# Kernel optimization log

Measured on AMD Instinct MI355X. Metric: run time of the kernel, lower is better.

## Reference

```python
import jax, jax.numpy as jnp
import numpy as np

EPS = 1e-5
PATCH_HW = 4096   # 64*64
STEP = 2048


def _conv(x, w, b=None, stride=(1, 1), pad=((0, 0), (0, 0))):
    y = jax.lax.conv_general_dilated(x, w, stride, pad,
                                     dimension_numbers=('NCHW', 'OIHW', 'NCHW'))
    return y if b is None else y + b[None, :, None, None]


def _bn(x, s, b, m, v):
    # inference-mode BatchNorm2d
    inv = s * jax.lax.rsqrt(v + EPS)
    return (x - m[None, :, None, None]) * inv[None, :, None, None] + b[None, :, None, None]


def _forward(x, w1, b1, w2, b2, w3, b3,
             c5a_w, bn5a_s, bn5a_b, bn5a_m, bn5a_v,
             c5c_w, bn5c_s, bn5c_b, bn5c_m, bn5c_v,
             c51_w, bn51_s, bn51_b, bn51_m, bn51_v,
             c52_w, bn52_s, bn52_b, bn52_m, bn52_v,
             pam_q_w, pam_q_b, pam_k_w, pam_k_b, pam_v_w, pam_v_b,
             pam_gamma, cam_gamma, c8_w, c8_b):
    B, L = x.shape
    need = PATCH_HW - (L % PATCH_HW)          # torch pads even when L%hw==0; L chosen non-multiple
    xp = jnp.pad(x, ((0, 0), (0, need)))
    nw = (xp.shape[1] - PATCH_HW) // STEP + 1  # sliding windows (unfold)
    idx = jnp.arange(nw)[:, None] * STEP + jnp.arange(PATCH_HW)[None, :]
    # [nw,1,64,64].reshape(1,1,hw,nw) in torch is a pure row-major reshape
    c_in = xp[:, idx].reshape(B, 1, PATCH_HW, nw)   # [B,1,4096,61]
    # FCN backbone
    h = jax.nn.relu(_conv(c_in, w1, b1, (4, 4), ((4, 4), (4, 4))))   # [B,128,1025,16]
    h = jax.nn.relu(_conv(h, w2, b2, (2, 2), ((2, 2), (2, 2))))      # [B,256,513,8]
    h = jax.nn.relu(_conv(h, w3, b3, (1, 1), ((1, 1), (1, 1))))      # [B,128,513,8]
    p1 = ((1, 1), (1, 1))
    # PAM branch
    feat1 = jax.nn.relu(_bn(_conv(h, c5a_w, None, (1, 1), p1), bn5a_s, bn5a_b, bn5a_m, bn5a_v))
    _, C, Hh, Ww = feat1.shape
    N = Hh * Ww                                    # 4104
    q = _conv(feat1, pam_q_w, pam_q_b).reshape(B, -1, N)   # [B,4,N]
    k = _conv(feat1, pam_k_w, pam_k_b).reshape(B, -1, N)
    attn = jax.nn.softmax(jnp.einsum('bdn,bdm->bnm', q, k), axis=-1)   # [B,N,N], no scaling (as in source)
    v = _conv(feat1, pam_v_w, pam_v_b).reshape(B, C, N)
    sa = pam_gamma * jnp.einsum('bcj,bij->bci', v, attn).reshape(feat1.shape) + feat1
    sa_conv = jax.nn.relu(_bn(_conv(sa, c51_w, None, (1, 1), p1), bn51_s, bn51_b, bn51_m, bn51_v))
    # CAM branch
    feat2 = jax.nn.relu(_bn(_conv(h, c5c_w, None, (1, 1), p1), bn5c_s, bn5c_b, bn5c_m, bn5c_v))
    Xf = feat2.reshape(B, C, N)
    energy = jnp.einsum('bcn,bdn->bcd', Xf, Xf)                 # [B,C,C]
    cattn = jax.nn.softmax(jnp.max(energy, -1, keepdims=True) - energy, axis=-1)  # max-subtract inversion
    sc = cam_gamma * jnp.einsum('bcd,bdn->bcn', cattn, Xf).reshape(feat2.shape) + feat2
    sc_conv = jax.nn.relu(_bn(_conv(sc, c52_w, None, (1, 1), p1), bn52_s, bn52_b, bn52_m, bn52_v))
    # fused head output (conv8; dropout is identity in eval)
    out = _conv(sa_conv + sc_conv, c8_w, c8_b)                  # [B,nclass,513,8]
    return out[:, None]                                          # torch.stack adds a dim -> [B,1,nclass,513,8]


def setup_inputs() -> dict:
    key = jax.random.key(0)
    it = iter(jax.random.split(key, 40))
    def rn(shape, s=0.05):
        return jax.random.normal(next(it), shape, jnp.float32) * s
    d = {}
    d['x'] = jax.random.normal(next(it), (4, 126975), jnp.float32)
    d['w1'] = rn((128, 1, 8, 8));   d['b1'] = rn((128,))
    d['w2'] = rn((256, 128, 5, 5)); d['b2'] = rn((256,))
    d['w3'] = rn((128, 256, 3, 3)); d['b3'] = rn((128,))
    for tag, cin in (('5a', 128), ('5c', 128), ('51', 32), ('52', 32)):
        d['c' + tag + '_w'] = rn((32, cin, 3, 3))
        d['bn' + tag + '_s'] = jnp.ones((32,), jnp.float32)
        d['bn' + tag + '_b'] = jnp.zeros((32,), jnp.float32)
        d['bn' + tag + '_m'] = jnp.zeros((32,), jnp.float32)
        d['bn' + tag + '_v'] = jnp.ones((32,), jnp.float32)
    d['pam_q_w'] = rn((4, 32, 1, 1));  d['pam_q_b'] = rn((4,))
    d['pam_k_w'] = rn((4, 32, 1, 1));  d['pam_k_b'] = rn((4,))
    d['pam_v_w'] = rn((32, 32, 1, 1)); d['pam_v_b'] = rn((32,))
    d['pam_gamma'] = jnp.array([0.5], jnp.float32)  # nonzero so attention path is live
    d['cam_gamma'] = jnp.array([0.5], jnp.float32)
    d['c8_w'] = rn((2, 32, 1, 1)); d['c8_b'] = rn((2,))
    return d


def reference(x, w1, b1, w2, b2, w3, b3,
              c5a_w, bn5a_s, bn5a_b, bn5a_m, bn5a_v,
              c5c_w, bn5c_s, bn5c_b, bn5c_m, bn5c_v,
              c51_w, bn51_s, bn51_b, bn51_m, bn51_v,
              c52_w, bn52_s, bn52_b, bn52_m, bn52_v,
              pam_q_w, pam_q_b, pam_k_w, pam_k_b, pam_v_w, pam_v_b,
              pam_gamma, cam_gamma, c8_w, c8_b):
    return _forward(x, w1, b1, w2, b2, w3, b3,
                    c5a_w, bn5a_s, bn5a_b, bn5a_m, bn5a_v,
                    c5c_w, bn5c_s, bn5c_b, bn5c_m, bn5c_v,
                    c51_w, bn51_s, bn51_b, bn51_m, bn51_v,
                    c52_w, bn52_s, bn52_b, bn52_m, bn52_v,
                    pam_q_w, pam_q_b, pam_k_w, pam_k_b, pam_v_w, pam_v_b,
                    pam_gamma, cam_gamma, c8_w, c8_b)
```

## Files before the change

kernel.cpp:

```cpp
#include <hip/hip_runtime.h>
#include <cstddef>

constexpr int BB   = 4;
constexpr int LX   = 126975;
constexpr int H0   = 4096, W0 = 61;
constexpr int C1   = 128, H1 = 1025, W1 = 16;
constexpr int C2   = 256, H2 = 513,  W2 = 8;
constexpr int C3   = 128;
constexpr int NN   = H2 * W2;
constexpr int NSPLIT = 15;
constexpr int JSPAN  = 288;
constexpr int NPAD   = 4104;

constexpr size_t SZ_H1    = (size_t)BB * C1 * H1 * W1;
constexpr size_t SZ_P2    = (size_t)BB * C2 * NN;
constexpr size_t SZ_F     = (size_t)BB * 32 * NN;
constexpr size_t SZ_QK    = (size_t)BB * 4 * NN;
constexpr size_t SZ_ACCP  = (size_t)NSPLIT * BB * 32 * NPAD;
constexpr size_t SZ_ML    = (size_t)NSPLIT * BB * 2 * NPAD;

constexpr size_t OFF_H1   = 0;
constexpr size_t OFF_P3   = 0;
constexpr size_t OFF_ACCP = 0;
constexpr size_t OFF_ML   = OFF_ACCP + SZ_ACCP;
constexpr size_t RB       = SZ_H1;
constexpr size_t OFF_P2   = RB;
constexpr size_t OFF_F1   = RB;
constexpr size_t OFF_F2   = OFF_F1 + SZ_F;
constexpr size_t OFF_Q    = OFF_F2 + SZ_F;
constexpr size_t OFF_K    = OFF_Q  + SZ_QK;
constexpr size_t OFF_V    = OFF_K  + SZ_QK;
constexpr size_t OFF_SA   = OFF_V  + SZ_F;
constexpr size_t OFF_SC   = OFF_SA + SZ_F;
constexpr size_t OFF_EN   = RB + SZ_P2;

__device__ __forceinline__ float frelu(float x) { return x > 0.f ? x : 0.f; }

__global__ __launch_bounds__(256) void k_conv1(const float* __restrict__ x,
                                               const float* __restrict__ w1,
                                               const float* __restrict__ b1,
                                               float* __restrict__ h1) {
  __shared__ __align__(16) float tile[68 * 68];
  const int oh0 = blockIdx.x * 16;
  const int oc0 = blockIdx.y * 8;
  const int b   = blockIdx.z;
  const int tid = threadIdx.x;
  const int ih0 = oh0 * 4 - 4;
  for (int e = tid; e < 68 * 68; e += 256) {
    int row = e / 68, col = e - row * 68;
    int ih = ih0 + row, iw = col - 4;
    float v = 0.f;
    if (ih >= 0 && ih < H0 && iw >= 0 && iw < W0) {
      int l   = ih * W0 + iw;
      int pos = (l >> 12) * 2048 + (l & 4095);
      if (pos < LX) v = x[(size_t)b * LX + pos];
    }
    tile[e] = v;
  }
  __syncthreads();
  const int oh_l = tid >> 4, ow = tid & 15;
  float acc[8];
#pragma unroll
  for (int o = 0; o < 8; ++o) acc[o] = 0.f;
#pragma unroll
  for (int kh = 0; kh < 8; ++kh) {
    const float* rp = &tile[(4 * oh_l + kh) * 68 + 4 * ow];
    float4 a0 = *(const float4*)rp;
    float4 a1 = *(const float4*)(rp + 4);
    float r[8] = {a0.x, a0.y, a0.z, a0.w, a1.x, a1.y, a1.z, a1.w};
#pragma unroll
    for (int kw = 0; kw < 8; ++kw) {
#pragma unroll
      for (int o = 0; o < 8; ++o)
        acc[o] = fmaf(r[kw], w1[(oc0 + o) * 64 + kh * 8 + kw], acc[o]);
    }
  }
  const int oh = oh0 + oh_l;
  if (oh < H1) {
#pragma unroll
    for (int o = 0; o < 8; ++o) {
      float v = frelu(acc[o] + b1[oc0 + o]);
      h1[(((size_t)b * C1 + oc0 + o) * H1 + oh) * W1 + ow] = v;
    }
  }
}

__global__ __launch_bounds__(256) void k_conv2(const float* __restrict__ h1,
                                               const float* __restrict__ w2,
                                               const float* __restrict__ b2,
                                               float* __restrict__ p2) {
  __shared__ __align__(16) float tin[4 * 19 * 20];
  __shared__ __align__(16) float twt[100 * 66];
  const int oh0 = blockIdx.x * 8;
  const int oc0 = blockIdx.y * 64;
  const int b   = blockIdx.z;
  const int tid = threadIdx.x;
  const int oh_l = tid & 7, ocg = tid >> 3;
  float acc[2][8] = {};
  for (int cc = 0; cc < 32; ++cc) {
    __syncthreads();
    for (int e = tid; e < 4 * 19 * 16; e += 256) {
      int ci = e / 304, r = e - ci * 304;
      int tr = r >> 4, c = r & 15;
      int ih = oh0 * 2 - 2 + tr;
      int cin = cc * 4 + ci;
      float v = 0.f;
      if (ih >= 0 && ih < H1) v = h1[(((size_t)b * C1 + cin) * H1 + ih) * W1 + c];
      tin[(ci * 19 + tr) * 20 + c] = v;
    }
    for (int e = tid; e < 6400; e += 256) {
      int oc_l = e / 100, t = e - oc_l * 100;
      twt[t * 66 + oc_l] = w2[(size_t)(oc0 + oc_l) * 3200 + cc * 100 + t];
    }
    __syncthreads();
#pragma unroll 1
    for (int ci = 0; ci < 4; ++ci) {
#pragma unroll
      for (int kh = 0; kh < 5; ++kh) {
        const float* rp = &tin[(ci * 19 + 2 * oh_l + kh) * 20];
        float4 a0 = *(const float4*)rp;
        float4 a1 = *(const float4*)(rp + 4);
        float4 a2 = *(const float4*)(rp + 8);
        float4 a3 = *(const float4*)(rp + 12);
        float rr[19];
        rr[0] = 0.f; rr[1] = 0.f; rr[18] = 0.f;
        rr[2] = a0.x; rr[3] = a0.y; rr[4] = a0.z; rr[5] = a0.w;
        rr[6] = a1.x; rr[7] = a1.y; rr[8] = a1.z; rr[9] = a1.w;
        rr[10] = a2.x; rr[11] = a2.y; rr[12] = a2.z; rr[13] = a2.w;
        rr[14] = a3.x; rr[15] = a3.y; rr[16] = a3.z; rr[17] = a3.w;
#pragma unroll
        for (int kw = 0; kw < 5; ++kw) {
          float2 wv = *(const float2*)&twt[(ci * 25 + kh * 5 + kw) * 66 + ocg * 2];
#pragma unroll
          for (int ow = 0; ow < 8; ++ow) {
            float r = rr[2 * ow + kw];
            acc[0][ow] = fmaf(r, wv.x, acc[0][ow]);
            acc[1][ow] = fmaf(r, wv.y, acc[1][ow]);
          }
        }
      }
    }
  }
  const int oh = oh0 + oh_l;
  if (oh < H2) {
#pragma unroll
    for (int o = 0; o < 2; ++o) {
      int oc = oc0 + ocg * 2 + o;
      float bo = b2[oc];
      float* dst = &p2[((size_t)b * C2 + oc) * NN + oh * 8];
      *(float4*)dst       = make_float4(frelu(acc[o][0] + bo), frelu(acc[o][1] + bo),
                                        frelu(acc[o][2] + bo), frelu(acc[o][3] + bo));
      *(float4*)(dst + 4) = make_float4(frelu(acc[o][4] + bo), frelu(acc[o][5] + bo),
                                        frelu(acc[o][6] + bo), frelu(acc[o][7] + bo));
    }
  }
}

__global__ __launch_bounds__(256) void k_conv3(const float* __restrict__ p2,
                                               const float* __restrict__ w3,
                                               const float* __restrict__ b3,
                                               float* __restrict__ p3) {
  __shared__ __align__(16) float tin[8 * 10 * 12];
  __shared__ __align__(16) float twt[72 * 66];
  const int oh0 = blockIdx.x * 8;
  const int oc0 = blockIdx.y * 64;
  const int b   = blockIdx.z;
  const int tid = threadIdx.x;
  const int oh_l = tid & 7, ocg = tid >> 3;
  float acc[2][8] = {};
  for (int cc = 0; cc < 32; ++cc) {
    __syncthreads();
    for (int e = tid; e < 640; e += 256) {
      int ci = e / 80, r = e - ci * 80;
      int tr = r >> 3, c = r & 7;
      int ih = oh0 - 1 + tr;
      int cin = cc * 8 + ci;
      float v = 0.f;
      if (ih >= 0 && ih < H2) v = p2[((size_t)b * C2 + cin) * NN + ih * 8 + c];
      tin[(ci * 10 + tr) * 12 + c] = v;
    }
    for (int e = tid; e < 4608; e += 256) {
      int oc_l = e / 72, t = e - oc_l * 72;
      twt[t * 66 + oc_l] = w3[(size_t)(oc0 + oc_l) * 2304 + cc * 72 + t];
    }
    __syncthreads();
#pragma unroll 1
    for (int ci = 0; ci < 8; ++ci) {
#pragma unroll
      for (int kh = 0; kh < 3; ++kh) {
        const float* rp = &tin[(ci * 10 + oh_l + kh) * 12];
        float4 a0 = *(const float4*)rp;
        float4 a1 = *(const float4*)(rp + 4);
        float rr[10];
        rr[0] = 0.f; rr[9] = 0.f;
        rr[1] = a0.x; rr[2] = a0.y; rr[3] = a0.z; rr[4] = a0.w;
        rr[5] = a1.x; rr[6] = a1.y; rr[7] = a1.z; rr[8] = a1.w;
#pragma unroll
        for (int kw = 0; kw < 3; ++kw) {
          float2 wv = *(const float2*)&twt[(ci * 9 + kh * 3 + kw) * 66 + ocg * 2];
#pragma unroll
          for (int ow = 0; ow < 8; ++ow) {
            float r = rr[ow + kw];
            acc[0][ow] = fmaf(r, wv.x, acc[0][ow]);
            acc[1][ow] = fmaf(r, wv.y, acc[1][ow]);
          }
        }
      }
    }
  }
  const int oh = oh0 + oh_l;
  if (oh < H2) {
#pragma unroll
    for (int o = 0; o < 2; ++o) {
      int oc = oc0 + ocg * 2 + o;
      float bo = b3[oc];
      float* dst = &p3[((size_t)b * C3 + oc) * NN + oh * 8];
      *(float4*)dst       = make_float4(frelu(acc[o][0] + bo), frelu(acc[o][1] + bo),
                                        frelu(acc[o][2] + bo), frelu(acc[o][3] + bo));
      *(float4*)(dst + 4) = make_float4(frelu(acc[o][4] + bo), frelu(acc[o][5] + bo),
                                        frelu(acc[o][6] + bo), frelu(acc[o][7] + bo));
    }
  }
}

__global__ __launch_bounds__(128) void k_c5(const float* __restrict__ p3,
                                            const float* __restrict__ wa,
                                            const float* __restrict__ sa5, const float* __restrict__ ba5,
                                            const float* __restrict__ ma5, const float* __restrict__ va5,
                                            const float* __restrict__ wc,
                                            const float* __restrict__ sc5, const float* __restrict__ bc5,
                                            const float* __restrict__ mc5, const float* __restrict__ vc5,
                                            float* __restrict__ f1, float* __restrict__ f2) {
  __shared__ __align__(16) float tin[8 * 10 * 12];
  __shared__ __align__(16) float twt[72 * 64];
  const int oh0 = blockIdx.x * 8;
  const int b   = blockIdx.y;
  const int tid = threadIdx.x;
  const int vocg = tid >> 3, oh_l = tid & 7;
  float acc[4][8] = {};
  for (int cc = 0; cc < 16; ++cc) {
    __syncthreads();
    for (int e = tid; e < 640; e += 128) {
      int ci = e / 80, r = e - ci * 80;
      int tr = r >> 3, c = r & 7;
      int ih = oh0 - 1 + tr;
      int cin = cc * 8 + ci;
      float v = 0.f;
      if (ih >= 0 && ih < H2) v = p3[((size_t)b * C3 + cin) * NN + ih * 8 + c];
      tin[(ci * 10 + tr) * 12 + c] = v;
    }
    for (int e = tid; e < 4608; e += 128) {
      int voc_l = e & 63, t = e >> 6;
      const float* base = (voc_l < 32) ? (wa + (size_t)voc_l * 1152) : (wc + (size_t)(voc_l - 32) * 1152);
      twt[t * 64 + voc_l] = base[cc * 8 * 9 + t];
    }
    __syncthreads();
#pragma unroll 1
    for (int ci = 0; ci < 8; ++ci) {
#pragma unroll
      for (int kh = 0; kh < 3; ++kh) {
        const float* rp = &tin[(ci * 10 + oh_l + kh) * 12];
        float4 a0 = *(const float4*)rp;
        float4 a1 = *(const float4*)(rp + 4);
        float rr[10];
        rr[0] = 0.f; rr[9] = 0.f;
        rr[1] = a0.x; rr[2] = a0.y; rr[3] = a0.z; rr[4] = a0.w;
        rr[5] = a1.x; rr[6] = a1.y; rr[7] = a1.z; rr[8] = a1.w;
#pragma unroll
        for (int kw = 0; kw < 3; ++kw) {
          float4 wv = *(const float4*)&twt[(ci * 9 + kh * 3 + kw) * 64 + vocg * 4];
#pragma unroll
          for (int ow = 0; ow < 8; ++ow) {
            float r = rr[ow + kw];
            acc[0][ow] = fmaf(r, wv.x, acc[0][ow]);
            acc[1][ow] = fmaf(r, wv.y, acc[1][ow]);
            acc[2][ow] = fmaf(r, wv.z, acc[2][ow]);
            acc[3][ow] = fmaf(r, wv.w, acc[3][ow]);
          }
        }
      }
    }
  }
  const int oh = oh0 + oh_l;
  if (oh < H2) {
#pragma unroll
    for (int vv = 0; vv < 4; ++vv) {
      int voc = vocg * 4 + vv;
      bool A = voc < 32;
      int ci = voc & 31;
      float sN = A ? sa5[ci] : sc5[ci];
      float bN = A ? ba5[ci] : bc5[ci];
      float mN = A ? ma5[ci] : mc5[ci];
      float vN = A ? va5[ci] : vc5[ci];
      float inv = sN * rsqrtf(vN + 1e-5f);
      float sh  = bN - mN * inv;
      float* dst = (A ? f1 : f2) + ((size_t)b * 32 + ci) * NN + oh * 8;
      float y[8];
#pragma unroll
      for (int ow = 0; ow < 8; ++ow) y[ow] = frelu(acc[vv][ow] * inv + sh);
      *(float4*)dst       = make_float4(y[0], y[1], y[2], y[3]);
      *(float4*)(dst + 4) = make_float4(y[4], y[5], y[6], y[7]);
    }
  }
}

__global__ __launch_bounds__(256) void k_qkv(const float* __restrict__ f1,
                                             const float* __restrict__ qw, const float* __restrict__ qbv,
                                             const float* __restrict__ kwp, const float* __restrict__ kbv,
                                             const float* __restrict__ vwp, const float* __restrict__ vbv,
                                             float* __restrict__ qo, float* __restrict__ ko,
                                             float* __restrict__ vo) {
  const int n = blockIdx.x * 256 + threadIdx.x;
  if (n >= NN) return;
  const int ocv = blockIdx.y, b = blockIdx.z;
  const float* w;
  float bias;
  float* dst;
  if (ocv < 4)      { w = qw + ocv * 32;        bias = qbv[ocv];     dst = qo + ((size_t)b * 4 + ocv) * NN; }
  else if (ocv < 8) { int o = ocv - 4; w = kwp + o * 32; bias = kbv[o]; dst = ko + ((size_t)b * 4 + o) * NN; }
  else              { int o = ocv - 8; w = vwp + o * 32; bias = vbv[o]; dst = vo + ((size_t)b * 32 + o) * NN; }
  float a = bias;
#pragma unroll
  for (int c = 0; c < 32; ++c) a = fmaf(f1[((size_t)b * 32 + c) * NN + n], w[c], a);
  dst[n] = a;
}

__device__ __forceinline__ float rmax32(const float (&p)[32]) {
  float x0 = p[0], x1 = p[1], x2 = p[2], x3 = p[3];
#pragma unroll
  for (int j = 4; j < 32; j += 4) {
    x0 = fmaxf(x0, p[j]); x1 = fmaxf(x1, p[j + 1]);
    x2 = fmaxf(x2, p[j + 2]); x3 = fmaxf(x3, p[j + 3]);
  }
  return fmaxf(fmaxf(x0, x1), fmaxf(x2, x3));
}
__device__ __forceinline__ float rsum32(const float (&p)[32]) {
  float x0 = p[0], x1 = p[1], x2 = p[2], x3 = p[3];
#pragma unroll
  for (int j = 4; j < 32; j += 4) { x0 += p[j]; x1 += p[j + 1]; x2 += p[j + 2]; x3 += p[j + 3]; }
  return (x0 + x1) + (x2 + x3);
}

__global__ __launch_bounds__(256) void k_flash(const float* __restrict__ qb,
                                               const float* __restrict__ kb,
                                               const float* __restrict__ vb,
                                               float* __restrict__ accp,
                                               float* __restrict__ mlb) {
  __shared__ __align__(16) float ks[4 * 32];
  __shared__ __align__(16) float vs[32 * 32];
  const int tid = threadIdx.x;
  const int ia  = blockIdx.x * 256 + tid;
  const int sp  = blockIdx.y;
  const int b   = blockIdx.z;
  float q[4];
#pragma unroll
  for (int d = 0; d < 4; ++d)
    q[d] = (ia < NN) ? qb[((size_t)b * 4 + d) * NN + ia] : 0.f;
  float m = -1e30f, l = 0.f;
  float acc[32];
#pragma unroll
  for (int c = 0; c < 32; ++c) acc[c] = 0.f;
  const int jbeg = sp * JSPAN;
  const int jend = (jbeg + JSPAN < NN) ? jbeg + JSPAN : NN;
  const int cs = tid >> 3, j4 = (tid & 7) * 4;
  for (int j0 = jbeg; j0 < jend; j0 += 32) {
    const int nv = (jend - j0 < 32) ? jend - j0 : 32;
    __syncthreads();
    {
      const float* vsrc = &vb[((size_t)b * 32 + cs) * NN + j0 + j4];
      float4 v4;
      if (j4 + 4 <= nv) {
        v4 = *(const float4*)vsrc;
      } else {
        v4.x = (j4 + 0 < nv) ? vsrc[0] : 0.f;
        v4.y = (j4 + 1 < nv) ? vsrc[1] : 0.f;
        v4.z = (j4 + 2 < nv) ? vsrc[2] : 0.f;
        v4.w = (j4 + 3 < nv) ? vsrc[3] : 0.f;
      }
      *(float4*)&vs[cs * 32 + j4] = v4;
      if (tid < 32) {
        const int d = tid >> 3;
        const float* ksrc = &kb[((size_t)b * 4 + d) * NN + j0 + j4];
        float4 k4;
        if (j4 + 4 <= nv) {
          k4 = *(const float4*)ksrc;
        } else {
          k4.x = (j4 + 0 < nv) ? ksrc[0] : 0.f;
          k4.y = (j4 + 1 < nv) ? ksrc[1] : 0.f;
          k4.z = (j4 + 2 < nv) ? ksrc[2] : 0.f;
          k4.w = (j4 + 3 < nv) ? ksrc[3] : 0.f;
        }
        *(float4*)&ks[d * 32 + j4] = k4;
      }
    }
    __syncthreads();
    float p[32];
#pragma unroll
    for (int jj = 0; jj < 8; ++jj) {
      float4 k0 = *(const float4*)&ks[0 * 32 + 4 * jj];
      float4 k1 = *(const float4*)&ks[1 * 32 + 4 * jj];
      float4 k2 = *(const float4*)&ks[2 * 32 + 4 * jj];
      float4 k3 = *(const float4*)&ks[3 * 32 + 4 * jj];
      p[4 * jj + 0] = fmaf(q[0], k0.x, fmaf(q[1], k1.x, fmaf(q[2], k2.x, q[3] * k3.x)));
      p[4 * jj + 1] = fmaf(q[0], k0.y, fmaf(q[1], k1.y, fmaf(q[2], k2.y, q[3] * k3.y)));
      p[4 * jj + 2] = fmaf(q[0], k0.z, fmaf(q[1], k1.z, fmaf(q[2], k2.z, q[3] * k3.z)));
      p[4 * jj + 3] = fmaf(q[0], k0.w, fmaf(q[1], k1.w, fmaf(q[2], k2.w, q[3] * k3.w)));
    }
    if (nv < 32) {
#pragma unroll
      for (int j = 0; j < 32; ++j)
        if (j >= nv) p[j] = -1e30f;
    }
    float mn = fmaxf(m, rmax32(p));
    float f = __expf(m - mn);
    m = mn;
#pragma unroll
    for (int j = 0; j < 32; ++j) p[j] = __expf(p[j] - mn);
    l = fmaf(l, f, rsum32(p));
#pragma unroll
    for (int c = 0; c < 32; ++c) acc[c] *= f;
#pragma unroll
    for (int jj = 0; jj < 8; ++jj) {
      float4 p4 = make_float4(p[4 * jj], p[4 * jj + 1], p[4 * jj + 2], p[4 * jj + 3]);
#pragma unroll
      for (int c = 0; c < 32; ++c) {
        float4 vv = *(const float4*)&vs[c * 32 + 4 * jj];
        acc[c] = fmaf(p4.x, vv.x, fmaf(p4.y, vv.y, fmaf(p4.z, vv.z, fmaf(p4.w, vv.w, acc[c]))));
      }
    }
  }
  if (ia < NN) {
    const size_t sb4 = (size_t)(sp * 4 + b);
#pragma unroll
    for (int c = 0; c < 32; ++c)
      accp[(sb4 * 32 + c) * NPAD + ia] = acc[c];
    mlb[(sb4 * 2 + 0) * NPAD + ia] = m;
    mlb[(sb4 * 2 + 1) * NPAD + ia] = l;
  }
}

__global__ __launch_bounds__(256) void k_combine(const float* __restrict__ accp,
                                                 const float* __restrict__ mlb,
                                                 const float* __restrict__ f1,
                                                 const float* __restrict__ gamma,
                                                 float* __restrict__ sa) {
  const int n = blockIdx.x * 256 + threadIdx.x;
  if (n >= NN) return;
  const int c = blockIdx.y, b = blockIdx.z;
  float m[NSPLIT], l[NSPLIT];
#pragma unroll
  for (int s = 0; s < NSPLIT; ++s) {
    m[s] = mlb[((size_t)(s * 4 + b) * 2 + 0) * NPAD + n];
    l[s] = mlb[((size_t)(s * 4 + b) * 2 + 1) * NPAD + n];
  }
  float ms = m[0];
#pragma unroll
  for (int s = 1; s < NSPLIT; ++s) ms = fmaxf(ms, m[s]);
  float den = 0.f, num = 0.f;
#pragma unroll
  for (int s = 0; s < NSPLIT; ++s) {
    float w = __expf(m[s] - ms);
    den = fmaf(l[s], w, den);
    num = fmaf(w, accp[((size_t)(s * 4 + b) * 32 + c) * NPAD + n], num);
  }
  size_t o = ((size_t)b * 32 + c) * NN + n;
  sa[o] = gamma[0] * num / den + f1[o];
}

__global__ __launch_bounds__(256) void k_zero(float* __restrict__ p) {
  int i = blockIdx.x * 256 + threadIdx.x;
  if (i < 4096) p[i] = 0.f;
}

__global__ __launch_bounds__(256) void k_energy(const float* __restrict__ f2,
                                                float* __restrict__ energy) {
  __shared__ float fs[32 * 257];
  const int n0 = blockIdx.x * 256, b = blockIdx.y, tid = threadIdx.x;
  for (int e = tid; e < 32 * 256; e += 256) {
    int c = e >> 8, nl = e & 255;
    int n = n0 + nl;
    fs[c * 257 + nl] = (n < NN) ? f2[((size_t)b * 32 + c) * NN + n] : 0.f;
  }
  __syncthreads();
  const int cg = tid >> 4, dg = tid & 15;
  const int c0 = cg * 2, d0 = dg * 2;
  float e00 = 0.f, e01 = 0.f, e10 = 0.f, e11 = 0.f;
  for (int t = 0; t < 256; ++t) {
    float a0 = fs[c0 * 257 + t], a1 = fs[(c0 + 1) * 257 + t];
    float b0 = fs[d0 * 257 + t], b1 = fs[(d0 + 1) * 257 + t];
    e00 = fmaf(a0, b0, e00); e01 = fmaf(a0, b1, e01);
    e10 = fmaf(a1, b0, e10); e11 = fmaf(a1, b1, e11);
  }
  float* eb = energy + b * 1024;
  atomicAdd(&eb[c0 * 32 + d0], e00);
  atomicAdd(&eb[c0 * 32 + d0 + 1], e01);
  atomicAdd(&eb[(c0 + 1) * 32 + d0], e10);
  atomicAdd(&eb[(c0 + 1) * 32 + d0 + 1], e11);
}

__global__ __launch_bounds__(64) void k_cam(const float* __restrict__ f2,
                                            const float* __restrict__ energy,
                                            const float* __restrict__ gamma,
                                            float* __restrict__ sc) {
  __shared__ __align__(16) float cat[32 * 32];
  const int lane = threadIdx.x, b = blockIdx.y;
  const int n = blockIdx.x * 64 + lane;
  if (lane < 32) {
    const float* eb = energy + b * 1024 + lane * 32;
    float e[32];
#pragma unroll
    for (int d = 0; d < 32; ++d) e[d] = eb[d];
    float mn = e[0];
#pragma unroll
    for (int d = 1; d < 32; ++d) mn = fminf(mn, e[d]);
    float w[32];
    float sum = 0.f;
#pragma unroll
    for (int d = 0; d < 32; ++d) { w[d] = __expf(mn - e[d]); sum += w[d]; }
    float inv = 1.f / sum;
#pragma unroll
    for (int d = 0; d < 32; ++d) cat[lane * 32 + d] = w[d] * inv;
  }
  __syncthreads();
  const bool ok = n < NN;
  float f[32];
#pragma unroll
  for (int c = 0; c < 32; ++c) f[c] = ok ? f2[((size_t)b * 32 + c) * NN + n] : 0.f;
  const float g = gamma[0];
#pragma unroll
  for (int c = 0; c < 32; ++c) {
    float a = 0.f;
#pragma unroll
    for (int k4 = 0; k4 < 8; ++k4) {
      float4 cw = *(const float4*)&cat[c * 32 + 4 * k4];
      a = fmaf(cw.x, f[4 * k4], fmaf(cw.y, f[4 * k4 + 1], fmaf(cw.z, f[4 * k4 + 2], fmaf(cw.w, f[4 * k4 + 3], a))));
    }
    if (ok) sc[((size_t)b * 32 + c) * NN + n] = g * a + f[c];
  }
}

__global__ __launch_bounds__(128) void k_final(const float* __restrict__ sa,
                                               const float* __restrict__ sc,
                                               const float* __restrict__ w51,
                                               const float* __restrict__ s51, const float* __restrict__ b51,
                                               const float* __restrict__ m51, const float* __restrict__ v51,
                                               const float* __restrict__ w52,
                                               const float* __restrict__ s52, const float* __restrict__ b52,
                                               const float* __restrict__ m52, const float* __restrict__ v52,
                                               const float* __restrict__ w8, const float* __restrict__ b8,
                                               float* __restrict__ out) {
  __shared__ __align__(16) float tin[2 * 8 * 10 * 12];
  __shared__ __align__(16) float twt[72 * 64];
  __shared__ float tmid[64 * 65];
  const int oh0 = blockIdx.x * 8;
  const int b   = blockIdx.y;
  const int tid = threadIdx.x;
  const int vocg = tid >> 3, oh_l = tid & 7;
  float acc[4][8] = {};
  for (int cc = 0; cc < 4; ++cc) {
    __syncthreads();
    for (int e = tid; e < 1280; e += 128) {
      int which = (e >= 640) ? 1 : 0;
      int r1 = e - which * 640;
      int ci = r1 / 80, r2 = r1 - ci * 80;
      int tr = r2 >> 3, c = r2 & 7;
      int ih = oh0 - 1 + tr;
      int cin = cc * 8 + ci;
      const float* src = which ? sc : sa;
      float v = 0.f;
      if (ih >= 0 && ih < H2) v = src[((size_t)b * 32 + cin) * NN + ih * 8 + c];
      tin[which * 960 + (ci * 10 + tr) * 12 + c] = v;
    }
    for (int e = tid; e < 4608; e += 128) {
      int voc_l = e & 63, t = e >> 6;
      const float* base = (voc_l < 32) ? (w51 + voc_l * 288) : (w52 + (voc_l - 32) * 288);
      twt[t * 64 + voc_l] = base[cc * 8 * 9 + t];
    }
    __syncthreads();
    const float* tbase = tin + (vocg < 8 ? 0 : 960);
#pragma unroll 1
    for (int ci = 0; ci < 8; ++ci) {
#pragma unroll
      for (int kh = 0; kh < 3; ++kh) {
        const float* rp = tbase + (ci * 10 + oh_l + kh) * 12;
        float4 a0 = *(const float4*)rp;
        float4 a1 = *(const float4*)(rp + 4);
        float rr[10];
        rr[0] = 0.f; rr[9] = 0.f;
        rr[1] = a0.x; rr[2] = a0.y; rr[3] = a0.z; rr[4] = a0.w;
        rr[5] = a1.x; rr[6] = a1.y; rr[7] = a1.z; rr[8] = a1.w;
#pragma unroll
        for (int kw = 0; kw < 3; ++kw) {
          float4 wv = *(const float4*)&twt[(ci * 9 + kh * 3 + kw) * 64 + vocg * 4];
#pragma unroll
          for (int ow = 0; ow < 8; ++ow) {
            float r = rr[ow + kw];
            acc[0][ow] = fmaf(r, wv.x, acc[0][ow]);
            acc[1][ow] = fmaf(r, wv.y, acc[1][ow]);
            acc[2][ow] = fmaf(r, wv.z, acc[2][ow]);
            acc[3][ow] = fmaf(r, wv.w, acc[3][ow]);
          }
        }
      }
    }
  }
  {
    float inv[4], sh[4];
#pragma unroll
    for (int vv = 0; vv < 4; ++vv) {
      int voc = vocg * 4 + vv;
      bool A = voc < 32;
      int ci = voc & 31;
      float sN = A ? s51[ci] : s52[ci];
      float bN = A ? b51[ci] : b52[ci];
      float mN = A ? m51[ci] : m52[ci];
      float vN = A ? v51[ci] : v52[ci];
      inv[vv] = sN * rsqrtf(vN + 1e-5f);
      sh[vv] = bN - mN * inv[vv];
    }
#pragma unroll
    for (int ow = 0; ow < 8; ++ow) {
      int pos = oh_l * 8 + ow;
#pragma unroll
      for (int vv = 0; vv < 4; ++vv) {
        float y = acc[vv][ow] * inv[vv] + sh[vv];
        tmid[pos * 65 + vocg * 4 + vv] = frelu(y);
      }
    }
  }
  __syncthreads();
  {
    const int o = tid >> 6, pos = tid & 63;
    const int oh = oh0 + (pos >> 3), ow = pos & 7;
    float a = b8[o];
    const float* wrow = w8 + o * 32;
#pragma unroll
    for (int c = 0; c < 32; ++c)
      a = fmaf(tmid[pos * 65 + c] + tmid[pos * 65 + 32 + c], wrow[c], a);
    if (oh < H2) out[((size_t)b * 2 + o) * NN + oh * 8 + ow] = a;
  }
}

extern "C" void kernel_launch(void* const* d_in, const int* in_sizes, int n_in,
                              void* d_out, int out_size, void* d_ws, size_t ws_size,
                              hipStream_t stream) {
  (void)in_sizes; (void)n_in; (void)out_size; (void)ws_size;
  const float* x      = (const float*)d_in[0];
  const float* w1     = (const float*)d_in[1];
  const float* b1     = (const float*)d_in[2];
  const float* w2     = (const float*)d_in[3];
  const float* b2     = (const float*)d_in[4];
  const float* w3     = (const float*)d_in[5];
  const float* b3     = (const float*)d_in[6];
  const float* c5a_w  = (const float*)d_in[7];
  const float* bn5a_s = (const float*)d_in[8];
  const float* bn5a_b = (const float*)d_in[9];
  const float* bn5a_m = (const float*)d_in[10];
  const float* bn5a_v = (const float*)d_in[11];
  const float* c5c_w  = (const float*)d_in[12];
  const float* bn5c_s = (const float*)d_in[13];
  const float* bn5c_b = (const float*)d_in[14];
  const float* bn5c_m = (const float*)d_in[15];
  const float* bn5c_v = (const float*)d_in[16];
  const float* c51_w  = (const float*)d_in[17];
  const float* bn51_s = (const float*)d_in[18];
  const float* bn51_b = (const float*)d_in[19];
  const float* bn51_m = (const float*)d_in[20];
  const float* bn51_v = (const float*)d_in[21];
  const float* c52_w  = (const float*)d_in[22];
  const float* bn52_s = (const float*)d_in[23];
  const float* bn52_b = (const float*)d_in[24];
  const float* bn52_m = (const float*)d_in[25];
  const float* bn52_v = (const float*)d_in[26];
  const float* pam_qw = (const float*)d_in[27];
  const float* pam_qb = (const float*)d_in[28];
  const float* pam_kw = (const float*)d_in[29];
  const float* pam_kb = (const float*)d_in[30];
  const float* pam_vw = (const float*)d_in[31];
  const float* pam_vb = (const float*)d_in[32];
  const float* pgamma = (const float*)d_in[33];
  const float* cgamma = (const float*)d_in[34];
  const float* c8_w   = (const float*)d_in[35];
  const float* c8_b   = (const float*)d_in[36];

  float* W    = (float*)d_ws;
  float* h1   = W + OFF_H1;
  float* p2   = W + OFF_P2;
  float* p3   = W + OFF_P3;
  float* f1   = W + OFF_F1;
  float* f2   = W + OFF_F2;
  float* qbuf = W + OFF_Q;
  float* kbuf = W + OFF_K;
  float* vbuf = W + OFF_V;
  float* sab  = W + OFF_SA;
  float* scb  = W + OFF_SC;
  float* accp = W + OFF_ACCP;
  float* mlb  = W + OFF_ML;
  float* enb  = W + OFF_EN;
  float* outp = (float*)d_out;

  k_conv1<<<dim3(65, 16, 4), 256, 0, stream>>>(x, w1, b1, h1);
  k_conv2<<<dim3(65, 4, 4), 256, 0, stream>>>(h1, w2, b2, p2);
  k_conv3<<<dim3(65, 2, 4), 256, 0, stream>>>(p2, w3, b3, p3);
  k_c5<<<dim3(65, 4), 128, 0, stream>>>(p3,
                                        c5a_w, bn5a_s, bn5a_b, bn5a_m, bn5a_v,
                                        c5c_w, bn5c_s, bn5c_b, bn5c_m, bn5c_v,
                                        f1, f2);
  k_qkv<<<dim3(17, 40, 4), 256, 0, stream>>>(f1, pam_qw, pam_qb, pam_kw, pam_kb,
                                             pam_vw, pam_vb, qbuf, kbuf, vbuf);
  k_zero<<<dim3(16), 256, 0, stream>>>(enb);
  k_flash<<<dim3(17, NSPLIT, 4), 256, 0, stream>>>(qbuf, kbuf, vbuf, accp, mlb);
  k_energy<<<dim3(17, 4), 256, 0, stream>>>(f2, enb);
  k_combine<<<dim3(17, 32, 4), 256, 0, stream>>>(accp, mlb, f1, pgamma, sab);
  k_cam<<<dim3(65, 4), 64, 0, stream>>>(f2, enb, cgamma, scb);
  k_final<<<dim3(65, 4), 128, 0, stream>>>(sab, scb,
                                           c51_w, bn51_s, bn51_b, bn51_m, bn51_v,
                                           c52_w, bn52_s, bn52_b, bn52_m, bn52_v,
                                           c8_w, c8_b, outp);
}
```

Measured before the change: 1.549 ms.

## Pre-transpose conv weights, read from global, split conv3 input channels

A new kernel transposes the conv2 and conv3 weights into [k][oc] layout in workspace. The convs then read float4 weights straight from global/L2 instead of staging them through shared memory, and each thread computes four output channels with 128-thread blocks. conv3 is split in half along input channels so twice as many blocks run, and k_c5 sums the two partial outputs and applies bias and ReLU when it loads them. This removes the per-iteration weight staging and its sync cost, but adds a transpose launch, extra partial-sum traffic and uncached weight reads each iteration.

```diff
diff --git a/kernel.cpp b/kernel.cpp
--- a/kernel.cpp
+++ b/kernel.cpp
@@ -14,13 +14,15 @@
 
 constexpr size_t SZ_H1    = (size_t)BB * C1 * H1 * W1;
 constexpr size_t SZ_P2    = (size_t)BB * C2 * NN;
+constexpr size_t SZ_P3    = (size_t)BB * C3 * NN;
 constexpr size_t SZ_F     = (size_t)BB * 32 * NN;
 constexpr size_t SZ_QK    = (size_t)BB * 4 * NN;
 constexpr size_t SZ_ACCP  = (size_t)NSPLIT * BB * 32 * NPAD;
 constexpr size_t SZ_ML    = (size_t)NSPLIT * BB * 2 * NPAD;
 
 constexpr size_t OFF_H1   = 0;
-constexpr size_t OFF_P3   = 0;
+constexpr size_t OFF_P3A  = 0;
+constexpr size_t OFF_P3B  = SZ_P3;
 constexpr size_t OFF_ACCP = 0;
 constexpr size_t OFF_ML   = OFF_ACCP + SZ_ACCP;
 constexpr size_t RB       = SZ_H1;
@@ -33,8 +35,19 @@
 constexpr size_t OFF_SA   = OFF_V  + SZ_F;
 constexpr size_t OFF_SC   = OFF_SA + SZ_F;
 constexpr size_t OFF_EN   = RB + SZ_P2;
+constexpr size_t OFF_W2T  = OFF_EN + 4096;
+constexpr size_t OFF_W3T  = OFF_W2T + 819200;
 
 __device__ __forceinline__ float frelu(float x) { return x > 0.f ? x : 0.f; }
+
+__global__ __launch_bounds__(256) void k_wtrans(const float* __restrict__ w2,
+                                                const float* __restrict__ w3,
+                                                float* __restrict__ w2T,
+                                                float* __restrict__ w3T) {
+  const int k = blockIdx.x, oc = threadIdx.x;
+  w2T[(size_t)k * 256 + oc] = w2[(size_t)oc * 3200 + k];
+  if (k < 2304 && oc < 128) w3T[(size_t)k * 128 + oc] = w3[(size_t)oc * 2304 + k];
+}
 
 __global__ __launch_bounds__(256) void k_conv1(const float* __restrict__ x,
                                                const float* __restrict__ w1,
@@ -85,36 +98,33 @@
   }
 }
 
-__global__ __launch_bounds__(256) void k_conv2(const float* __restrict__ h1,
-                                               const float* __restrict__ w2,
+__global__ __launch_bounds__(128) void k_conv2(const float* __restrict__ h1,
+                                               const float* __restrict__ w2T,
                                                const float* __restrict__ b2,
                                                float* __restrict__ p2) {
   __shared__ __align__(16) float tin[4 * 19 * 20];
-  __shared__ __align__(16) float twt[100 * 66];
   const int oh0 = blockIdx.x * 8;
   const int oc0 = blockIdx.y * 64;
   const int b   = blockIdx.z;
   const int tid = threadIdx.x;
   const int oh_l = tid & 7, ocg = tid >> 3;
-  float acc[2][8] = {};
+  const int ih0 = oh0 * 2 - 2;
+  float acc[4][8] = {};
   for (int cc = 0; cc < 32; ++cc) {
     __syncthreads();
-    for (int e = tid; e < 4 * 19 * 16; e += 256) {
+    for (int e = tid; e < 4 * 19 * 16; e += 128) {
       int ci = e / 304, r = e - ci * 304;
       int tr = r >> 4, c = r & 15;
-      int ih = oh0 * 2 - 2 + tr;
+      int ih = ih0 + tr;
       int cin = cc * 4 + ci;
       float v = 0.f;
       if (ih >= 0 && ih < H1) v = h1[(((size_t)b * C1 + cin) * H1 + ih) * W1 + c];
       tin[(ci * 19 + tr) * 20 + c] = v;
     }
-    for (int e = tid; e < 6400; e += 256) {
-      int oc_l = e / 100, t = e - oc_l * 100;
-      twt[t * 66 + oc_l] = w2[(size_t)(oc0 + oc_l) * 3200 + cc * 100 + t];
-    }
     __syncthreads();
 #pragma unroll 1
     for (int ci = 0; ci < 4; ++ci) {
+      const float* wbase = &w2T[(size_t)((cc * 4 + ci) * 25) * 256 + oc0 + ocg * 4];
 #pragma unroll
       for (int kh = 0; kh < 5; ++kh) {
         const float* rp = &tin[(ci * 19 + 2 * oh_l + kh) * 20];
@@ -130,12 +140,14 @@
         rr[14] = a3.x; rr[15] = a3.y; rr[16] = a3.z; rr[17] = a3.w;
 #pragma unroll
         for (int kw = 0; kw < 5; ++kw) {
-          float2 wv = *(const float2*)&twt[(ci * 25 + kh * 5 + kw) * 66 + ocg * 2];
+          float4 wv = *(const float4*)&wbase[(kh * 5 + kw) * 256];
 #pragma unroll
           for (int ow = 0; ow < 8; ++ow) {
             float r = rr[2 * ow + kw];
             acc[0][ow] = fmaf(r, wv.x, acc[0][ow]);
             acc[1][ow] = fmaf(r, wv.y, acc[1][ow]);
+            acc[2][ow] = fmaf(r, wv.z, acc[2][ow]);
+            acc[3][ow] = fmaf(r, wv.w, acc[3][ow]);
           }
         }
       }
@@ -144,8 +156,8 @@
   const int oh = oh0 + oh_l;
   if (oh < H2) {
 #pragma unroll
-    for (int o = 0; o < 2; ++o) {
-      int oc = oc0 + ocg * 2 + o;
+    for (int o = 0; o < 4; ++o) {
+      int oc = oc0 + ocg * 4 + o;
       float bo = b2[oc];
       float* dst = &p2[((size_t)b * C2 + oc) * NN + oh * 8];
       *(float4*)dst       = make_float4(frelu(acc[o][0] + bo), frelu(acc[o][1] + bo),
@@ -156,36 +168,34 @@
   }
 }
 
-__global__ __launch_bounds__(256) void k_conv3(const float* __restrict__ p2,
-                                               const float* __restrict__ w3,
-                                               const float* __restrict__ b3,
-                                               float* __restrict__ p3) {
+__global__ __launch_bounds__(128) void k_conv3(const float* __restrict__ p2,
+                                               const float* __restrict__ w3T,
+                                               float* __restrict__ p3a,
+                                               float* __restrict__ p3b) {
   __shared__ __align__(16) float tin[8 * 10 * 12];
-  __shared__ __align__(16) float twt[72 * 66];
-  const int oh0 = blockIdx.x * 8;
-  const int oc0 = blockIdx.y * 64;
-  const int b   = blockIdx.z;
-  const int tid = threadIdx.x;
+  const int oh0  = blockIdx.x * 8;
+  const int oc0  = (blockIdx.y & 1) * 64;
+  const int half = blockIdx.y >> 1;
+  const int b    = blockIdx.z;
+  const int tid  = threadIdx.x;
   const int oh_l = tid & 7, ocg = tid >> 3;
-  float acc[2][8] = {};
-  for (int cc = 0; cc < 32; ++cc) {
-    __syncthreads();
-    for (int e = tid; e < 640; e += 256) {
+  float acc[4][8] = {};
+  float* outp = half ? p3b : p3a;
+  for (int cc = 0; cc < 16; ++cc) {
+    __syncthreads();
+    for (int e = tid; e < 640; e += 128) {
       int ci = e / 80, r = e - ci * 80;
       int tr = r >> 3, c = r & 7;
       int ih = oh0 - 1 + tr;
-      int cin = cc * 8 + ci;
+      int cin = half * 128 + cc * 8 + ci;
       float v = 0.f;
       if (ih >= 0 && ih < H2) v = p2[((size_t)b * C2 + cin) * NN + ih * 8 + c];
       tin[(ci * 10 + tr) * 12 + c] = v;
     }
-    for (int e = tid; e < 4608; e += 256) {
-      int oc_l = e / 72, t = e - oc_l * 72;
-      twt[t * 66 + oc_l] = w3[(size_t)(oc0 + oc_l) * 2304 + cc * 72 + t];
-    }
     __syncthreads();
 #pragma unroll 1
     for (int ci = 0; ci < 8; ++ci) {
+      const float* wbase = &w3T[(size_t)((half * 128 + cc * 8 + ci) * 9) * 128 + oc0 + ocg * 4];
 #pragma unroll
       for (int kh = 0; kh < 3; ++kh) {
         const float* rp = &tin[(ci * 10 + oh_l + kh) * 12];
@@ -197,12 +207,14 @@
         rr[5] = a1.x; rr[6] = a1.y; rr[7] = a1.z; rr[8] = a1.w;
 #pragma unroll
         for (int kw = 0; kw < 3; ++kw) {
-          float2 wv = *(const float2*)&twt[(ci * 9 + kh * 3 + kw) * 66 + ocg * 2];
+          float4 wv = *(const float4*)&wbase[(kh * 3 + kw) * 128];
 #pragma unroll
           for (int ow = 0; ow < 8; ++ow) {
             float r = rr[ow + kw];
             acc[0][ow] = fmaf(r, wv.x, acc[0][ow]);
             acc[1][ow] = fmaf(r, wv.y, acc[1][ow]);
+            acc[2][ow] = fmaf(r, wv.z, acc[2][ow]);
+            acc[3][ow] = fmaf(r, wv.w, acc[3][ow]);
           }
         }
       }
@@ -211,19 +223,18 @@
   const int oh = oh0 + oh_l;
   if (oh < H2) {
 #pragma unroll
-    for (int o = 0; o < 2; ++o) {
-      int oc = oc0 + ocg * 2 + o;
-      float bo = b3[oc];
-      float* dst = &p3[((size_t)b * C3 + oc) * NN + oh * 8];
-      *(float4*)dst       = make_float4(frelu(acc[o][0] + bo), frelu(acc[o][1] + bo),
-                                        frelu(acc[o][2] + bo), frelu(acc[o][3] + bo));
-      *(float4*)(dst + 4) = make_float4(frelu(acc[o][4] + bo), frelu(acc[o][5] + bo),
-                                        frelu(acc[o][6] + bo), frelu(acc[o][7] + bo));
-    }
-  }
-}
-
-__global__ __launch_bounds__(128) void k_c5(const float* __restrict__ p3,
+    for (int o = 0; o < 4; ++o) {
+      int oc = oc0 + ocg * 4 + o;
+      float* dst = &outp[((size_t)b * C3 + oc) * NN + oh * 8];
+      *(float4*)dst       = make_float4(acc[o][0], acc[o][1], acc[o][2], acc[o][3]);
+      *(float4*)(dst + 4) = make_float4(acc[o][4], acc[o][5], acc[o][6], acc[o][7]);
+    }
+  }
+}
+
+__global__ __launch_bounds__(128) void k_c5(const float* __restrict__ p3a,
+                                            const float* __restrict__ p3b,
+                                            const float* __restrict__ b3,
                                             const float* __restrict__ wa,
                                             const float* __restrict__ sa5, const float* __restrict__ ba5,
                                             const float* __restrict__ ma5, const float* __restrict__ va5,
@@ -246,7 +257,10 @@
       int ih = oh0 - 1 + tr;
       int cin = cc * 8 + ci;
       float v = 0.f;
-      if (ih >= 0 && ih < H2) v = p3[((size_t)b * C3 + cin) * NN + ih * 8 + c];
+      if (ih >= 0 && ih < H2) {
+        size_t idx = ((size_t)b * C3 + cin) * NN + ih * 8 + c;
+        v = frelu(p3a[idx] + p3b[idx] + b3[cin]);
+      }
       tin[(ci * 10 + tr) * 12 + c] = v;
     }
     for (int e = tid; e < 4608; e += 128) {
@@ -686,7 +700,8 @@
   float* W    = (float*)d_ws;
   float* h1   = W + OFF_H1;
   float* p2   = W + OFF_P2;
-  float* p3   = W + OFF_P3;
+  float* p3a  = W + OFF_P3A;
+  float* p3b  = W + OFF_P3B;
   float* f1   = W + OFF_F1;
   float* f2   = W + OFF_F2;
   float* qbuf = W + OFF_Q;
@@ -697,12 +712,15 @@
   float* accp = W + OFF_ACCP;
   float* mlb  = W + OFF_ML;
   float* enb  = W + OFF_EN;
+  float* w2T  = W + OFF_W2T;
+  float* w3T  = W + OFF_W3T;
   float* outp = (float*)d_out;
 
+  k_wtrans<<<dim3(3200), 256, 0, stream>>>(w2, w3, w2T, w3T);
   k_conv1<<<dim3(65, 16, 4), 256, 0, stream>>>(x, w1, b1, h1);
-  k_conv2<<<dim3(65, 4, 4), 256, 0, stream>>>(h1, w2, b2, p2);
-  k_conv3<<<dim3(65, 2, 4), 256, 0, stream>>>(p2, w3, b3, p3);
-  k_c5<<<dim3(65, 4), 128, 0, stream>>>(p3,
+  k_conv2<<<dim3(65, 4, 4), 128, 0, stream>>>(h1, w2T, b2, p2);
+  k_conv3<<<dim3(65, 4, 4), 128, 0, stream>>>(p2, w3T, p3a, p3b);
+  k_c5<<<dim3(65, 4), 128, 0, stream>>>(p3a, p3b, b3,
                                         c5a_w, bn5a_s, bn5a_b, bn5a_m, bn5a_v,
                                         c5c_w, bn5c_s, bn5c_b, bn5c_m, bn5c_v,
                                         f1, f2);
```

Result: slower. 1.581 ms (+2.0%).
